# Performance work log

Hardware: AMD Instinct MI355X
Metric: run time of the kernel (lower is better)

The kernel has to match this reference:

```python
import jax, jax.numpy as jnp
import numpy as np

IN_CH, OUT_CH, B, H, W = 32, 64, 8, 256, 256
EPS = 1e-5

SOBEL_X = [[1., 0., -1.], [2., 0., -2.], [1., 0., -1.]]
SOBEL_Y = [[1., 2., 1.], [0., 0., 0.], [-1., -2., -1.]]
LAP = [[0., 1., 0.], [1., -4., 1.], [0., 1., 0.]]

DN = ('NCHW', 'OIHW', 'NCHW')


def conv2d(x, w, b, pad, groups=1):
    y = jax.lax.conv_general_dilated(x, w, (1, 1), [(pad, pad), (pad, pad)],
                                     dimension_numbers=DN, feature_group_count=groups)
    return y + b[None, :, None, None]


def dw_conv(x, k2d):
    # fixed depthwise 3x3 conv, groups=C, padding=1, no bias
    c = x.shape[1]
    kern = jnp.tile(jnp.asarray(k2d, x.dtype)[None, None], (c, 1, 1, 1))  # (C,1,3,3)
    return jax.lax.conv_general_dilated(x, kern, (1, 1), [(1, 1), (1, 1)],
                                        dimension_numbers=DN, feature_group_count=c)


def bn4d(x, p):  # eval-mode BN; x (B,C,H,W), p (4,C) = gamma, beta, mean, var
    g, b, m, v = p
    s = g * jax.lax.rsqrt(v + EPS)
    return (x - m[None, :, None, None]) * s[None, :, None, None] + b[None, :, None, None]


def bn2d(h, p):  # h (B,C)
    g, b, m, v = p
    return (h - m) * (g * jax.lax.rsqrt(v + EPS)) + b


def _bn_params(key, c):
    k1, k2, k3, k4 = jax.random.split(key, 4)
    g = 1.0 + 0.1 * jax.random.normal(k1, (c,), jnp.float32)
    b = 0.1 * jax.random.normal(k2, (c,), jnp.float32)
    m = 0.1 * jax.random.normal(k3, (c,), jnp.float32)
    v = jax.random.uniform(k4, (c,), jnp.float32, 0.5, 1.5)
    return jnp.stack([g, b, m, v])


def setup_inputs() -> dict:
    key = jax.random.key(0)
    ks = jax.random.split(key, 24)
    s = 0.05
    return {
        'x': jax.random.normal(ks[0], (B, IN_CH, H, W), jnp.float32),
        'gate_w1': s * jax.random.normal(ks[1], (IN_CH, IN_CH), jnp.float32),
        'gate_b1': s * jax.random.normal(ks[2], (IN_CH,), jnp.float32),
        'gate_bn': _bn_params(ks[3], IN_CH),
        'gate_w2': s * jax.random.normal(ks[4], (3, IN_CH), jnp.float32),
        'gate_b2': s * jax.random.normal(ks[5], (3,), jnp.float32),
        'mw1': s * jax.random.normal(ks[6], (OUT_CH, IN_CH, 3, 3), jnp.float32),
        'mb1': s * jax.random.normal(ks[7], (OUT_CH,), jnp.float32),
        'mbn1': _bn_params(ks[8], OUT_CH),
        'mw2': s * jax.random.normal(ks[9], (OUT_CH, OUT_CH, 5, 5), jnp.float32),
        'mb2': s * jax.random.normal(ks[10], (OUT_CH,), jnp.float32),
        'mbn2': _bn_params(ks[11], OUT_CH),
        'sxw': s * jax.random.normal(ks[12], (OUT_CH, IN_CH, 5, 5), jnp.float32),
        'sxb': s * jax.random.normal(ks[13], (OUT_CH,), jnp.float32),
        'sxbn': _bn_params(ks[14], OUT_CH),
        'syw': s * jax.random.normal(ks[15], (OUT_CH, IN_CH, 5, 5), jnp.float32),
        'syb': s * jax.random.normal(ks[16], (OUT_CH,), jnp.float32),
        'sybn': _bn_params(ks[17], OUT_CH),
        'lw': s * jax.random.normal(ks[18], (OUT_CH, IN_CH, 5, 5), jnp.float32),
        'lb': s * jax.random.normal(ks[19], (OUT_CH,), jnp.float32),
        'lbn': _bn_params(ks[20], OUT_CH),
    }


def reference(x, gate_w1, gate_b1, gate_bn, gate_w2, gate_b2,
              mw1, mb1, mbn1, mw2, mb2, mbn2,
              sxw, sxb, sxbn, syw, syb, sybn, lw, lb, lbn):
    # gate: GAP -> 1x1 conv -> BN -> tanh -> 1x1 conv -> top-1 one-hot over 3 experts
    gap = x.mean((2, 3))                                   # (B, C_in)
    h = jnp.tanh(bn2d(gap @ gate_w1.T + gate_b1, gate_bn))
    k = h @ gate_w2.T + gate_b2                            # (B, 3)
    oh = jax.nn.one_hot(jnp.argmax(k, axis=1), 3, dtype=x.dtype)  # (B, 3)

    # expert 0: main branch (conv3x3+BN+ReLU -> conv5x5+BN+ReLU)
    main = jax.nn.relu(bn4d(conv2d(x, mw1, mb1, 1), mbn1))
    main = jax.nn.relu(bn4d(conv2d(main, mw2, mb2, 2), mbn2))

    # expert 1: mean of sobel-x and sobel-y branches
    sx = jax.nn.relu(bn4d(conv2d(dw_conv(x, SOBEL_X), sxw, sxb, 2), sxbn))
    sy = jax.nn.relu(bn4d(conv2d(dw_conv(x, SOBEL_Y), syw, syb, 2), sybn))
    sobel = (sx + sy) * 0.5

    # expert 2: laplacian branch
    lap = jax.nn.relu(bn4d(conv2d(dw_conv(x, LAP), lw, lb, 2), lbn))

    # one-hot gated combination (== stack + one_hot mask + sum in the original)
    w = oh[:, :, None, None, None]  # (B, 3, 1, 1, 1)
    return main * w[:, 0] + sobel * w[:, 1] + lap * w[:, 2]
```

## Files before the change

### kernel.cpp

```cpp
#include <hip/hip_runtime.h>

#define BB 8
#define IC 32
#define OC 64
#define HH 256
#define WW 256
#define EPS 1e-5f

typedef __attribute__((ext_vector_type(8))) short bf16x8;
typedef __attribute__((ext_vector_type(4))) float f32x4;

#define YSTR 40
#define XSTR 40

#define WS_GAP   0
#define WS_BIDX  256
#define WS_W1F   264
#define WS_B1F   (WS_W1F + 9216)
#define WS_W2F   (WS_B1F + 64)
#define WS_B2F   (WS_W2F + 51200)
#define WS_SXWT  (WS_B2F + 64)
#define WS_SXBF  (WS_SXWT + 51200)
#define WS_SYWT  (WS_SXBF + 64)
#define WS_SYBF  (WS_SYWT + 51200)
#define WS_LWT   (WS_SYBF + 64)
#define WS_LBF   (WS_LWT + 51200)
#define WS_XT    (WS_LBF + 64)
#define WS_ZPAD  (WS_XT + 8388608)
#define WS_NEED_FAST ((size_t)(WS_ZPAD + 16) * 4)

__device__ inline unsigned short bf16r(float f) {
    unsigned int u = __float_as_uint(f);
    unsigned int r = (u + 0x7fffu + ((u >> 16) & 1u)) >> 16;
    return (unsigned short)r;
}

__device__ __forceinline__ void gld16(const void* g, const void* l) {
    __builtin_amdgcn_global_load_lds(
        (const __attribute__((address_space(1))) void*)(unsigned long long)(g),
        (__attribute__((address_space(3))) void*)(unsigned int)(unsigned long long)(l),
        16, 0, 0);
}

__global__ void prep_kernel(const float* __restrict__ mw1, const float* __restrict__ mb1, const float* __restrict__ mbn1,
                            const float* __restrict__ mw2, const float* __restrict__ mb2, const float* __restrict__ mbn2,
                            const float* __restrict__ sxw, const float* __restrict__ sxb, const float* __restrict__ sxbn,
                            const float* __restrict__ syw, const float* __restrict__ syb, const float* __restrict__ sybn,
                            const float* __restrict__ lw,  const float* __restrict__ lb,  const float* __restrict__ lbn,
                            float* __restrict__ ws, int fast) {
    int idx = blockIdx.x * 256 + threadIdx.x;

    if (idx < 18432) {
        int j = idx & 7, lane = (idx >> 3) & 63, oct = (idx >> 9) & 1, ht = idx >> 10;
        int t = ht % 9, h = ht / 9;
        int oc = h * 32 + oct * 16 + (lane & 15);
        int ic = (lane >> 4) * 8 + j;
        float s = mbn1[oc] * rsqrtf(mbn1[192 + oc] + EPS);
        ((unsigned short*)(ws + WS_W1F))[idx] = bf16r(mw1[(oc * IC + ic) * 9 + t] * s);
    }
    if (idx < 102400) {
        int j = idx & 7, lane = (idx >> 3) & 63, oct = (idx >> 9) & 3, ht = idx >> 11;
        int t = ht % 25, h = ht / 25;
        int oc = oct * 16 + (lane & 15);
        int ic = h * 32 + (lane >> 4) * 8 + j;
        float s = mbn2[oc] * rsqrtf(mbn2[192 + oc] + EPS);
        ((unsigned short*)(ws + WS_W2F))[idx] = bf16r(mw2[(oc * OC + ic) * 25 + t] * s);
    }
    if (idx < 51200) {
        int oc = idx & 63, k = (idx >> 6) % 25, ic = idx / (25 * 64);
        float ssx = sxbn[oc] * rsqrtf(sxbn[192 + oc] + EPS);
        float ssy = sybn[oc] * rsqrtf(sybn[192 + oc] + EPS);
        float sl  = lbn[oc]  * rsqrtf(lbn[192 + oc]  + EPS);
        ws[WS_SXWT + idx] = sxw[(oc * IC + ic) * 25 + k] * ssx;
        ws[WS_SYWT + idx] = syw[(oc * IC + ic) * 25 + k] * ssy;
        ws[WS_LWT  + idx] = lw [(oc * IC + ic) * 25 + k] * sl;
    }
    if (idx < 256) ws[WS_GAP + idx] = 0.f;
    if (fast && idx < 16) ws[WS_ZPAD + idx] = 0.f;
    if (idx < 64) {
        float s1 = mbn1[idx] * rsqrtf(mbn1[192 + idx] + EPS);
        ws[WS_B1F + idx] = (mb1[idx] - mbn1[128 + idx]) * s1 + mbn1[64 + idx];
        float s2 = mbn2[idx] * rsqrtf(mbn2[192 + idx] + EPS);
        ws[WS_B2F + idx] = (mb2[idx] - mbn2[128 + idx]) * s2 + mbn2[64 + idx];
        float sx = sxbn[idx] * rsqrtf(sxbn[192 + idx] + EPS);
        ws[WS_SXBF + idx] = (sxb[idx] - sxbn[128 + idx]) * sx + sxbn[64 + idx];
        float sy = sybn[idx] * rsqrtf(sybn[192 + idx] + EPS);
        ws[WS_SYBF + idx] = (syb[idx] - sybn[128 + idx]) * sy + sybn[64 + idx];
        float sl = lbn[idx] * rsqrtf(lbn[192 + idx] + EPS);
        ws[WS_LBF + idx] = (lb[idx] - lbn[128 + idx]) * sl + lbn[64 + idx];
    }
}

__global__ void __launch_bounds__(256, 2)
xform_kernel(const float* __restrict__ x, float* __restrict__ ws) {
    int b = blockIdx.y, row = blockIdx.x, t = threadIdx.x;
    const float* xb = x + (size_t)b * (IC * HH * WW) + (size_t)row * WW;

    unsigned int pk[16];
    #pragma unroll
    for (int k = 0; k < 32; k += 2) {
        float v0 = xb[(size_t)k * (HH * WW) + t];
        float v1 = xb[(size_t)(k + 1) * (HH * WW) + t];
        pk[k >> 1] = (unsigned int)bf16r(v0) | ((unsigned int)bf16r(v1) << 16);
    }
    short* xt = (short*)(ws + WS_XT) + ((size_t)b * (HH * WW) + (size_t)row * WW + t) * 32;
    uint4* dp = (uint4*)xt;
    dp[0] = make_uint4(pk[0],  pk[1],  pk[2],  pk[3]);
    dp[1] = make_uint4(pk[4],  pk[5],  pk[6],  pk[7]);
    dp[2] = make_uint4(pk[8],  pk[9],  pk[10], pk[11]);
    dp[3] = make_uint4(pk[12], pk[13], pk[14], pk[15]);

    __shared__ float gl[32];
    int w = t >> 6, lane = t & 63;
    #pragma unroll
    for (int kk = 0; kk < 8; kk++) {
        int k = w * 8 + kk;
        const float* rp = xb + (size_t)k * (HH * WW);
        float s = rp[lane] + rp[lane + 64] + rp[lane + 128] + rp[lane + 192];
        #pragma unroll
        for (int off = 32; off; off >>= 1) s += __shfl_down(s, off, 64);
        if (lane == 0) gl[k] = s;
    }
    __syncthreads();
    if (t < 32) atomicAdd(ws + WS_GAP + b * 32 + t, gl[t] * (1.f / (HH * WW)));
}

__global__ void gap_kernel(const float* __restrict__ x, float* __restrict__ ws) {
    int bc = blockIdx.x;
    const float4* p = (const float4*)(x + (size_t)bc * (HH * WW));
    float s = 0.f;
    for (int i = threadIdx.x; i < (HH * WW) / 4; i += 256) {
        float4 v = p[i];
        s += (v.x + v.y) + (v.z + v.w);
    }
    #pragma unroll
    for (int off = 32; off; off >>= 1) s += __shfl_down(s, off, 64);
    __shared__ float red[4];
    int lane = threadIdx.x & 63, w = threadIdx.x >> 6;
    if (lane == 0) red[w] = s;
    __syncthreads();
    if (threadIdx.x == 0)
        ws[WS_GAP + bc] = (red[0] + red[1] + red[2] + red[3]) * (1.f / (HH * WW));
}

__global__ void gate_kernel(const float* __restrict__ w1, const float* __restrict__ b1,
                            const float* __restrict__ gbn,
                            const float* __restrict__ w2, const float* __restrict__ b2,
                            float* __restrict__ ws) {
    __shared__ float hsh[8][32];
    int tid = threadIdx.x;
    int b = tid >> 5, j = tid & 31;
    float acc = b1[j];
    for (int i = 0; i < 32; i++) acc += ws[WS_GAP + b * 32 + i] * w1[j * 32 + i];
    float s = gbn[j] * rsqrtf(gbn[96 + j] + EPS);
    hsh[b][j] = tanhf((acc - gbn[64 + j]) * s + gbn[32 + j]);
    __syncthreads();
    if (tid < 8) {
        float best = -1e30f; int bi = 0;
        for (int c = 0; c < 3; c++) {
            float k = b2[c];
            for (int jj = 0; jj < 32; jj++) k += hsh[tid][jj] * w2[c * 32 + jj];
            if (k > best) { best = k; bi = c; }
        }
        ((int*)ws)[WS_BIDX + tid] = bi;
    }
}

template <int ASYNC>
__global__ void __launch_bounds__(256, 2)
main_kernel(const float* __restrict__ x, const float* __restrict__ ws, float* __restrict__ out) {
    __shared__ __align__(1024) short xs[ASYNC ? 496 * 32 : 484 * XSTR];
    __shared__ __align__(16)   short ys[400 * YSTR];

    int b = blockIdx.y;
    if (((const int*)ws)[WS_BIDX + b] != 0) return;
    int tile = blockIdx.x;
    int ty = (tile >> 4) * 16, tx = (tile & 15) * 16;
    int tid = threadIdx.x;
    int w = tid >> 6, lane = tid & 63, n = lane & 15, quad = lane >> 4;

    if constexpr (ASYNC) {
        const short* xtb = (const short*)(ws + WS_XT) + (size_t)b * (HH * WW * 32);
        const void* zp = (const void*)(ws + WS_ZPAD);
        for (int c = w; c < 31; c += 4) {
            int D = c * 1024 + (lane << 4);
            int L = D ^ (((D >> 7) & 7) << 4);
            int pL = L >> 6, qL = (L >> 4) & 3;
            int rr = pL / 22, cc2 = pL - rr * 22;
            int gy = ty - 3 + rr, gx = tx - 3 + cc2;
            bool v = (pL < 484) && ((unsigned)gy < HH) && ((unsigned)gx < WW);
            const void* src = v ? (const void*)(xtb + (((gy << 8) + gx) * 32) + (qL << 3)) : zp;
            gld16(src, (const void*)((const char*)xs + c * 1024));
        }
    } else {
        const float* xb = x + (size_t)b * IC * HH * WW;
        for (int p = tid; p < 484; p += 256) {
            int rr = p / 22, cc = p % 22;
            int gy = ty - 3 + rr, gx = tx - 3 + cc;
            bool v = ((unsigned)gy < HH) && ((unsigned)gx < WW);
            const float* xp = xb + gy * WW + gx;
            short* dst = xs + p * XSTR;
            #pragma unroll
            for (int ic = 0; ic < IC; ic += 4) {
                float f0 = v ? xp[(size_t)(ic + 0) * (HH * WW)] : 0.f;
                float f1 = v ? xp[(size_t)(ic + 1) * (HH * WW)] : 0.f;
                float f2 = v ? xp[(size_t)(ic + 2) * (HH * WW)] : 0.f;
                float f3 = v ? xp[(size_t)(ic + 3) * (HH * WW)] : 0.f;
                uint2 pk;
                pk.x = (unsigned int)bf16r(f0) | ((unsigned int)bf16r(f1) << 16);
                pk.y = (unsigned int)bf16r(f2) | ((unsigned int)bf16r(f3) << 16);
                *(uint2*)(dst + ic) = pk;
            }
        }
    }

    auto ldb = [&](int P) -> bf16x8 {
        if constexpr (ASYNC) {
            int L = (P << 6) + (quad << 4);
            int A = L ^ (((L >> 7) & 7) << 4);
            return *(const bf16x8*)((const char*)xs + A);
        } else {
            return *(const bf16x8*)(xs + P * XSTR + quad * 8);
        }
    };

    const short* w1v = (const short*)(ws + WS_W1F);
    const bf16x8* w2v = (const bf16x8*)(ws + WS_W2F);

    f32x4 acc2[4][4];
    #pragma unroll
    for (int i = 0; i < 4; i++)
        #pragma unroll
        for (int jj = 0; jj < 4; jj++) acc2[i][jj] = (f32x4){0.f, 0.f, 0.f, 0.f};
    int mrow0 = w * 4;
    int yr0   = w * 5;

    __syncthreads();

    #pragma unroll 1
    for (int h = 0; h < 2; h++) {
        if (h) __syncthreads();

        #pragma unroll
        for (int cg = 0; cg < 2; cg++) {
            int cb = cg * 4;
            f32x4 a1[5][2];
            #pragma unroll
            for (int rr = 0; rr < 5; rr++) {
                a1[rr][0] = (f32x4){0.f, 0.f, 0.f, 0.f};
                a1[rr][1] = (f32x4){0.f, 0.f, 0.f, 0.f};
            }
            #pragma unroll
            for (int dw = 0; dw < 3; dw++) {
                bf16x8 w1f[3][2];
                #pragma unroll
                for (int dh = 0; dh < 3; dh++) {
                    int t = dh * 3 + dw;
                    w1f[dh][0] = *(const bf16x8*)(w1v + (((h * 9 + t) * 2 + 0) * 64 + lane) * 8);
                    w1f[dh][1] = *(const bf16x8*)(w1v + (((h * 9 + t) * 2 + 1) * 64 + lane) * 8);
                }
                bf16x8 bfr[7];
                #pragma unroll
                for (int rI = 0; rI < 7; rI++)
                    bfr[rI] = ldb((yr0 + rI) * 22 + cb + n + dw);
                #pragma unroll
                for (int dh = 0; dh < 3; dh++)
                    #pragma unroll
                    for (int rr = 0; rr < 5; rr++) {
                        a1[rr][0] = __builtin_amdgcn_mfma_f32_16x16x32_bf16(w1f[dh][0], bfr[rr + dh], a1[rr][0], 0, 0, 0);
                        a1[rr][1] = __builtin_amdgcn_mfma_f32_16x16x32_bf16(w1f[dh][1], bfr[rr + dh], a1[rr][1], 0, 0, 0);
                    }
            }
            #pragma unroll
            for (int oct = 0; oct < 2; oct++) {
                float bias1[4];
                #pragma unroll
                for (int r = 0; r < 4; r++)
                    bias1[r] = ws[WS_B1F + h * 32 + oct * 16 + quad * 4 + r];
                #pragma unroll
                for (int rr = 0; rr < 5; rr++) {
                    int yr = yr0 + rr;
                    int gy2 = ty - 2 + yr, gx2 = tx - 2 + cb + n;
                    bool inb = ((unsigned)gy2 < HH) && ((unsigned)gx2 < WW);
                    float v0 = inb ? fmaxf(a1[rr][oct][0] + bias1[0], 0.f) : 0.f;
                    float v1 = inb ? fmaxf(a1[rr][oct][1] + bias1[1], 0.f) : 0.f;
                    float v2 = inb ? fmaxf(a1[rr][oct][2] + bias1[2], 0.f) : 0.f;
                    float v3 = inb ? fmaxf(a1[rr][oct][3] + bias1[3], 0.f) : 0.f;
                    uint2 pkk;
                    pkk.x = (unsigned int)bf16r(v0) | ((unsigned int)bf16r(v1) << 16);
                    pkk.y = (unsigned int)bf16r(v2) | ((unsigned int)bf16r(v3) << 16);
                    *(uint2*)(ys + (yr * 20 + cb + n) * YSTR + oct * 16 + quad * 4) = pkk;
                }
            }
        }
        __syncthreads();

        const bf16x8* w2h = w2v + (size_t)h * 100 * 64;
        bf16x8 afq[4][4];
        #pragma unroll
        for (int kp = 0; kp < 4; kp++) {
            int tn = (kp % 5) * 5 + (kp / 5);
            int base = tn * 256 + lane;
            afq[kp][0] = w2h[base];       afq[kp][1] = w2h[base + 64];
            afq[kp][2] = w2h[base + 128]; afq[kp][3] = w2h[base + 192];
        }
        bf16x8 bfr2[8];
        #pragma unroll
        for (int k = 0; k < 25; k++) {
            int dw = k / 5, dh = k % 5;
            if (dh == 0) {
                #pragma unroll
                for (int rI = 0; rI < 8; rI++)
                    bfr2[rI] = *(const bf16x8*)(ys + ((mrow0 + rI) * 20 + n + dw) * YSTR + quad * 8);
            }
            #pragma unroll
            for (int r4 = 0; r4 < 4; r4++) {
                bf16x8 bb = bfr2[r4 + dh];
                acc2[r4][0] = __builtin_amdgcn_mfma_f32_16x16x32_bf16(afq[k & 3][0], bb, acc2[r4][0], 0, 0, 0);
                acc2[r4][1] = __builtin_amdgcn_mfma_f32_16x16x32_bf16(afq[k & 3][1], bb, acc2[r4][1], 0, 0, 0);
                acc2[r4][2] = __builtin_amdgcn_mfma_f32_16x16x32_bf16(afq[k & 3][2], bb, acc2[r4][2], 0, 0, 0);
                acc2[r4][3] = __builtin_amdgcn_mfma_f32_16x16x32_bf16(afq[k & 3][3], bb, acc2[r4][3], 0, 0, 0);
            }
            if (k + 4 < 25) {
                int kk = k + 4;
                int tn = (kk % 5) * 5 + (kk / 5);
                int base = tn * 256 + lane;
                afq[k & 3][0] = w2h[base];       afq[k & 3][1] = w2h[base + 64];
                afq[k & 3][2] = w2h[base + 128]; afq[k & 3][3] = w2h[base + 192];
            }
        }
    }

    float bias2[4][4];
    #pragma unroll
    for (int oct = 0; oct < 4; oct++)
        #pragma unroll
        for (int r = 0; r < 4; r++)
            bias2[oct][r] = ws[WS_B2F + oct * 16 + quad * 4 + r];

    float* ob = out + (size_t)b * OC * HH * WW;
    #pragma unroll
    for (int r4 = 0; r4 < 4; r4++) {
        int orow = mrow0 + r4;
        #pragma unroll
        for (int oct = 0; oct < 4; oct++) {
            #pragma unroll
            for (int r = 0; r < 4; r++) {
                int oc = oct * 16 + quad * 4 + r;
                float v = fmaxf(acc2[r4][oct][r] + bias2[oct][r], 0.f);
                ob[(size_t)oc * (HH * WW) + (ty + orow) * WW + tx + n] = v;
            }
        }
    }
}

__global__ void __launch_bounds__(256, 2)
edge_kernel(const float* __restrict__ x, const float* __restrict__ ws, float* __restrict__ out) {
    constexpr float KSX[9] = {1, 0, -1, 2, 0, -2, 1, 0, -1};
    constexpr float KSY[9] = {1, 2, 1, 0, 0, 0, -1, -2, -1};
    constexpr float KLP[9] = {0, 1, 0, 1, -4, 1, 0, 1, 0};

    __shared__ float xsf[8 * 484];
    __shared__ float ysf[8 * 400];
    int b = blockIdx.y;
    int sel = ((const int*)ws)[WS_BIDX + b];
    if (sel == 0) return;
    int npass = (sel == 1) ? 2 : 1;
    float scale = (sel == 1) ? 0.5f : 1.0f;

    int tile = blockIdx.x;
    int ty = (tile >> 4) * 16, tx = (tile & 15) * 16;
    int tid = threadIdx.x;
    const float* xb = x + (size_t)b * IC * HH * WW;

    int ocg = tid >> 5;
    int ps  = tid & 31;
    int row = ps >> 1, c0 = (ps & 1) * 8;

    for (int pass = 0; pass < npass; pass++) {
        int kid = (sel == 1) ? pass : 2;
        const float* wt = ws + (kid == 0 ? WS_SXWT : (kid == 1 ? WS_SYWT : WS_LWT));
        const float* bf = ws + (kid == 0 ? WS_SXBF : (kid == 1 ? WS_SYBF : WS_LBF));

        float acc[8][8];
        #pragma unroll
        for (int o = 0; o < 8; o++)
            #pragma unroll
            for (int j = 0; j < 8; j++) acc[o][j] = 0.f;

        for (int icc = 0; icc < 4; icc++) {
            if (icc || pass) __syncthreads();
            for (int i = tid; i < 8 * 484; i += 256) {
                int ch = i / 484, rem = i % 484, rr = rem / 22, cc = rem % 22;
                int ic = icc * 8 + ch;
                int gy = ty - 3 + rr, gx = tx - 3 + cc;
                float v = 0.f;
                if ((unsigned)gy < HH && (unsigned)gx < WW) v = xb[(size_t)ic * HH * WW + gy * WW + gx];
                xsf[i] = v;
            }
            __syncthreads();
            for (int p = tid; p < 400; p += 256) {
                int r = p / 20, c = p % 20;
                bool inb = ((unsigned)(ty - 2 + r) < HH) && ((unsigned)(tx - 2 + c) < WW);
                #pragma unroll
                for (int ch = 0; ch < 8; ch++) {
                    const float* xp = xsf + ch * 484 + r * 22 + c;
                    float v = 0.f;
                    #pragma unroll
                    for (int k = 0; k < 9; k++) {
                        float kv = (kid == 0) ? KSX[k] : (kid == 1) ? KSY[k] : KLP[k];
                        v += kv * xp[(k / 3) * 22 + (k % 3)];
                    }
                    ysf[ch * 400 + p] = inb ? v : 0.f;
                }
            }
            __syncthreads();
            for (int ic8 = 0; ic8 < 8; ic8++) {
                const float* yc = ysf + ic8 * 400;
                const float* wbase = wt + ((icc * 8 + ic8) * 25) * 64 + ocg * 8;
                #pragma unroll
                for (int dh = 0; dh < 5; dh++) {
                    #pragma unroll
                    for (int dw = 0; dw < 5; dw++) {
                        const float* yp = yc + (row + dh) * 20 + c0 + dw;
                        float yv[8];
                        #pragma unroll
                        for (int j = 0; j < 8; j++) yv[j] = yp[j];
                        const float4* wp = (const float4*)(wbase + (dh * 5 + dw) * 64);
                        float4 wa = wp[0], wb = wp[1];
                        float wr[8] = {wa.x, wa.y, wa.z, wa.w, wb.x, wb.y, wb.z, wb.w};
                        #pragma unroll
                        for (int o = 0; o < 8; o++)
                            #pragma unroll
                            for (int j = 0; j < 8; j++) acc[o][j] += wr[o] * yv[j];
                    }
                }
            }
        }
        float* ob = out + (size_t)b * OC * HH * WW;
        #pragma unroll
        for (int o = 0; o < 8; o++) {
            int oc = ocg * 8 + o;
            float bb = bf[oc];
            float* op = ob + (size_t)oc * HH * WW + (ty + row) * WW + tx + c0;
            if (pass) {
                #pragma unroll
                for (int j = 0; j < 8; j++) op[j] += scale * fmaxf(acc[o][j] + bb, 0.f);
            } else {
                #pragma unroll
                for (int j = 0; j < 8; j++) op[j] = scale * fmaxf(acc[o][j] + bb, 0.f);
            }
        }
    }
}

extern "C" void kernel_launch(void* const* d_in, const int* in_sizes, int n_in,
                              void* d_out, int out_size, void* d_ws, size_t ws_size,
                              hipStream_t stream) {
    const float* x    = (const float*)d_in[0];
    const float* gw1  = (const float*)d_in[1];
    const float* gb1  = (const float*)d_in[2];
    const float* gbn  = (const float*)d_in[3];
    const float* gw2  = (const float*)d_in[4];
    const float* gb2  = (const float*)d_in[5];
    const float* mw1  = (const float*)d_in[6];
    const float* mb1  = (const float*)d_in[7];
    const float* mbn1 = (const float*)d_in[8];
    const float* mw2  = (const float*)d_in[9];
    const float* mb2  = (const float*)d_in[10];
    const float* mbn2 = (const float*)d_in[11];
    const float* sxw  = (const float*)d_in[12];
    const float* sxb  = (const float*)d_in[13];
    const float* sxbn = (const float*)d_in[14];
    const float* syw  = (const float*)d_in[15];
    const float* syb  = (const float*)d_in[16];
    const float* sybn = (const float*)d_in[17];
    const float* lw   = (const float*)d_in[18];
    const float* lb   = (const float*)d_in[19];
    const float* lbn  = (const float*)d_in[20];
    float* ws  = (float*)d_ws;
    float* out = (float*)d_out;

    int fast = (ws_size >= WS_NEED_FAST) ? 1 : 0;

    prep_kernel<<<400, 256, 0, stream>>>(mw1, mb1, mbn1, mw2, mb2, mbn2,
                                         sxw, sxb, sxbn, syw, syb, sybn, lw, lb, lbn, ws, fast);
    if (fast) {
        xform_kernel<<<dim3(HH, BB), 256, 0, stream>>>(x, ws);
    } else {
        gap_kernel<<<256, 256, 0, stream>>>(x, ws);
    }
    gate_kernel<<<1, 256, 0, stream>>>(gw1, gb1, gbn, gw2, gb2, ws);

    dim3 grid(256, BB);
    if (fast) {
        main_kernel<1><<<grid, 256, 0, stream>>>(x, ws, out);
    } else {
        main_kernel<0><<<grid, 256, 0, stream>>>(x, ws, out);
    }
    edge_kernel<<<grid, 256, 0, stream>>>(x, ws, out);
}
```

Measured before the change: 435.4 us.

## Port edge-expert conv5x5 to bf16 MFMA with async transposed input staging

Rewrites the edge (sobel/laplacian) kernel so its 5x5 conv runs on bf16 MFMA instructions instead of scalar FP32 FMAs. Weights are pre-packed in prep as bf16 in MFMA fragment order. The input tile comes from the pre-transposed bf16 channels-last workspace via async global-to-LDS loads with swizzling. All 32 channels are staged at once, and both sobel passes are accumulated in registers before a single store, which removes the read-modify-write of the output. The cost is lower precision (bf16 inputs, depthwise results and weights) and higher register use for the two accumulator sets.

```diff
diff --git a/kernel.cpp b/kernel.cpp
--- a/kernel.cpp
+++ b/kernel.cpp
@@ -34,6 +34,9 @@
     unsigned int r = (u + 0x7fffu + ((u >> 16) & 1u)) >> 16;
     return (unsigned short)r;
 }
+__device__ inline float bf2f(unsigned short s) {
+    return __uint_as_float(((unsigned int)s) << 16);
+}
 
 __device__ __forceinline__ void gld16(const void* g, const void* l) {
     __builtin_amdgcn_global_load_lds(
@@ -67,13 +70,15 @@
         ((unsigned short*)(ws + WS_W2F))[idx] = bf16r(mw2[(oc * OC + ic) * 25 + t] * s);
     }
     if (idx < 51200) {
-        int oc = idx & 63, k = (idx >> 6) % 25, ic = idx / (25 * 64);
+        int j = idx & 7, lane = (idx >> 3) & 63, oct = (idx >> 9) & 3, t = idx >> 11;
+        int oc = oct * 16 + (lane & 15);
+        int ic = (lane >> 4) * 8 + j;
         float ssx = sxbn[oc] * rsqrtf(sxbn[192 + oc] + EPS);
         float ssy = sybn[oc] * rsqrtf(sybn[192 + oc] + EPS);
         float sl  = lbn[oc]  * rsqrtf(lbn[192 + oc]  + EPS);
-        ws[WS_SXWT + idx] = sxw[(oc * IC + ic) * 25 + k] * ssx;
-        ws[WS_SYWT + idx] = syw[(oc * IC + ic) * 25 + k] * ssy;
-        ws[WS_LWT  + idx] = lw [(oc * IC + ic) * 25 + k] * sl;
+        ((unsigned short*)(ws + WS_SXWT))[idx] = bf16r(sxw[(oc * IC + ic) * 25 + t] * ssx);
+        ((unsigned short*)(ws + WS_SYWT))[idx] = bf16r(syw[(oc * IC + ic) * 25 + t] * ssy);
+        ((unsigned short*)(ws + WS_LWT ))[idx] = bf16r(lw [(oc * IC + ic) * 25 + t] * sl);
     }
     if (idx < 256) ws[WS_GAP + idx] = 0.f;
     if (fast && idx < 16) ws[WS_ZPAD + idx] = 0.f;
@@ -354,101 +359,176 @@
     }
 }
 
+template <int ASYNC>
 __global__ void __launch_bounds__(256, 2)
 edge_kernel(const float* __restrict__ x, const float* __restrict__ ws, float* __restrict__ out) {
     constexpr float KSX[9] = {1, 0, -1, 2, 0, -2, 1, 0, -1};
     constexpr float KSY[9] = {1, 2, 1, 0, 0, 0, -1, -2, -1};
     constexpr float KLP[9] = {0, 1, 0, 1, -4, 1, 0, 1, 0};
 
-    __shared__ float xsf[8 * 484];
-    __shared__ float ysf[8 * 400];
+    __shared__ __align__(1024) short xs[ASYNC ? 496 * 32 : 484 * XSTR];
+    __shared__ __align__(16)   short ys[400 * YSTR];
+
     int b = blockIdx.y;
     int sel = ((const int*)ws)[WS_BIDX + b];
     if (sel == 0) return;
-    int npass = (sel == 1) ? 2 : 1;
-    float scale = (sel == 1) ? 0.5f : 1.0f;
-
     int tile = blockIdx.x;
     int ty = (tile >> 4) * 16, tx = (tile & 15) * 16;
     int tid = threadIdx.x;
-    const float* xb = x + (size_t)b * IC * HH * WW;
-
-    int ocg = tid >> 5;
-    int ps  = tid & 31;
-    int row = ps >> 1, c0 = (ps & 1) * 8;
-
+    int w = tid >> 6, lane = tid & 63, n = lane & 15, quad = lane >> 4;
+
+    if constexpr (ASYNC) {
+        const short* xtb = (const short*)(ws + WS_XT) + (size_t)b * (HH * WW * 32);
+        const void* zp = (const void*)(ws + WS_ZPAD);
+        for (int c = w; c < 31; c += 4) {
+            int D = c * 1024 + (lane << 4);
+            int L = D ^ (((D >> 7) & 7) << 4);
+            int pL = L >> 6, qL = (L >> 4) & 3;
+            int rr = pL / 22, cc2 = pL - rr * 22;
+            int gy = ty - 3 + rr, gx = tx - 3 + cc2;
+            bool v = (pL < 484) && ((unsigned)gy < HH) && ((unsigned)gx < WW);
+            const void* src = v ? (const void*)(xtb + (((gy << 8) + gx) * 32) + (qL << 3)) : zp;
+            gld16(src, (const void*)((const char*)xs + c * 1024));
+        }
+    } else {
+        const float* xb = x + (size_t)b * IC * HH * WW;
+        for (int p = tid; p < 484; p += 256) {
+            int rr = p / 22, cc = p % 22;
+            int gy = ty - 3 + rr, gx = tx - 3 + cc;
+            bool v = ((unsigned)gy < HH) && ((unsigned)gx < WW);
+            const float* xp = xb + gy * WW + gx;
+            short* dst = xs + p * XSTR;
+            #pragma unroll
+            for (int ic = 0; ic < IC; ic += 4) {
+                float f0 = v ? xp[(size_t)(ic + 0) * (HH * WW)] : 0.f;
+                float f1 = v ? xp[(size_t)(ic + 1) * (HH * WW)] : 0.f;
+                float f2 = v ? xp[(size_t)(ic + 2) * (HH * WW)] : 0.f;
+                float f3 = v ? xp[(size_t)(ic + 3) * (HH * WW)] : 0.f;
+                uint2 pk;
+                pk.x = (unsigned int)bf16r(f0) | ((unsigned int)bf16r(f1) << 16);
+                pk.y = (unsigned int)bf16r(f2) | ((unsigned int)bf16r(f3) << 16);
+                *(uint2*)(dst + ic) = pk;
+            }
+        }
+    }
+
+    auto ldq = [&](int P, int q) -> bf16x8 {
+        if constexpr (ASYNC) {
+            int L = (P << 6) + (q << 4);
+            int A = L ^ (((L >> 7) & 7) << 4);
+            return *(const bf16x8*)((const char*)xs + A);
+        } else {
+            return *(const bf16x8*)(xs + P * XSTR + q * 8);
+        }
+    };
+
+    int mrow0 = w * 4;
+    int npass = (sel == 1) ? 2 : 1;
+    f32x4 accA[4][4];
+    f32x4 acc2[4][4];
+
+    __syncthreads();
+
+    #pragma unroll 1
     for (int pass = 0; pass < npass; pass++) {
         int kid = (sel == 1) ? pass : 2;
-        const float* wt = ws + (kid == 0 ? WS_SXWT : (kid == 1 ? WS_SYWT : WS_LWT));
-        const float* bf = ws + (kid == 0 ? WS_SXBF : (kid == 1 ? WS_SYBF : WS_LBF));
-
-        float acc[8][8];
-        #pragma unroll
-        for (int o = 0; o < 8; o++)
-            #pragma unroll
-            for (int j = 0; j < 8; j++) acc[o][j] = 0.f;
-
-        for (int icc = 0; icc < 4; icc++) {
-            if (icc || pass) __syncthreads();
-            for (int i = tid; i < 8 * 484; i += 256) {
-                int ch = i / 484, rem = i % 484, rr = rem / 22, cc = rem % 22;
-                int ic = icc * 8 + ch;
-                int gy = ty - 3 + rr, gx = tx - 3 + cc;
-                float v = 0.f;
-                if ((unsigned)gy < HH && (unsigned)gx < WW) v = xb[(size_t)ic * HH * WW + gy * WW + gx];
-                xsf[i] = v;
-            }
-            __syncthreads();
-            for (int p = tid; p < 400; p += 256) {
-                int r = p / 20, c = p % 20;
-                bool inb = ((unsigned)(ty - 2 + r) < HH) && ((unsigned)(tx - 2 + c) < WW);
-                #pragma unroll
-                for (int ch = 0; ch < 8; ch++) {
-                    const float* xp = xsf + ch * 484 + r * 22 + c;
-                    float v = 0.f;
+        if (pass) __syncthreads();
+
+        for (int t2 = tid; t2 < 1600; t2 += 256) {
+            int q = t2 & 3, px = t2 >> 2;
+            int pr = px / 20, pc = px - pr * 20;
+            bool inb = ((unsigned)(ty - 2 + pr) < HH) && ((unsigned)(tx - 2 + pc) < WW);
+            float a[8] = {0.f, 0.f, 0.f, 0.f, 0.f, 0.f, 0.f, 0.f};
+            if (inb) {
+                #pragma unroll
+                for (int dr = 0; dr < 3; dr++)
                     #pragma unroll
-                    for (int k = 0; k < 9; k++) {
-                        float kv = (kid == 0) ? KSX[k] : (kid == 1) ? KSY[k] : KLP[k];
-                        v += kv * xp[(k / 3) * 22 + (k % 3)];
+                    for (int dc = 0; dc < 3; dc++) {
+                        float kv = (kid == 0) ? KSX[dr * 3 + dc]
+                                 : (kid == 1) ? KSY[dr * 3 + dc]
+                                              : KLP[dr * 3 + dc];
+                        if (kv != 0.f) {
+                            bf16x8 v = ldq((pr + dr) * 22 + pc + dc, q);
+                            #pragma unroll
+                            for (int j = 0; j < 8; j++)
+                                a[j] += kv * bf2f((unsigned short)v[j]);
+                        }
                     }
-                    ysf[ch * 400 + p] = inb ? v : 0.f;
+            }
+            uint4 pk;
+            pk.x = (unsigned int)bf16r(a[0]) | ((unsigned int)bf16r(a[1]) << 16);
+            pk.y = (unsigned int)bf16r(a[2]) | ((unsigned int)bf16r(a[3]) << 16);
+            pk.z = (unsigned int)bf16r(a[4]) | ((unsigned int)bf16r(a[5]) << 16);
+            pk.w = (unsigned int)bf16r(a[6]) | ((unsigned int)bf16r(a[7]) << 16);
+            *(uint4*)(ys + px * YSTR + q * 8) = pk;
+        }
+        __syncthreads();
+
+        #pragma unroll
+        for (int i = 0; i < 4; i++)
+            #pragma unroll
+            for (int jj = 0; jj < 4; jj++) acc2[i][jj] = (f32x4){0.f, 0.f, 0.f, 0.f};
+
+        const bf16x8* wf = (const bf16x8*)(ws + (kid == 0 ? WS_SXWT : kid == 1 ? WS_SYWT : WS_LWT));
+        bf16x8 afq[2][4];
+        #pragma unroll
+        for (int kp = 0; kp < 2; kp++) {
+            int tn = kp * 5;
+            int base = tn * 256 + lane;
+            afq[kp][0] = wf[base];       afq[kp][1] = wf[base + 64];
+            afq[kp][2] = wf[base + 128]; afq[kp][3] = wf[base + 192];
+        }
+        bf16x8 bfr2[8];
+        #pragma unroll
+        for (int k = 0; k < 25; k++) {
+            int dw = k / 5, dh = k % 5;
+            if (dh == 0) {
+                #pragma unroll
+                for (int rI = 0; rI < 8; rI++)
+                    bfr2[rI] = *(const bf16x8*)(ys + ((mrow0 + rI) * 20 + n + dw) * YSTR + quad * 8);
+            }
+            #pragma unroll
+            for (int r4 = 0; r4 < 4; r4++) {
+                bf16x8 bb = bfr2[r4 + dh];
+                acc2[r4][0] = __builtin_amdgcn_mfma_f32_16x16x32_bf16(afq[k & 1][0], bb, acc2[r4][0], 0, 0, 0);
+                acc2[r4][1] = __builtin_amdgcn_mfma_f32_16x16x32_bf16(afq[k & 1][1], bb, acc2[r4][1], 0, 0, 0);
+                acc2[r4][2] = __builtin_amdgcn_mfma_f32_16x16x32_bf16(afq[k & 1][2], bb, acc2[r4][2], 0, 0, 0);
+                acc2[r4][3] = __builtin_amdgcn_mfma_f32_16x16x32_bf16(afq[k & 1][3], bb, acc2[r4][3], 0, 0, 0);
+            }
+            if (k + 2 < 25) {
+                int kk = k + 2;
+                int tn = (kk % 5) * 5 + (kk / 5);
+                int base = tn * 256 + lane;
+                afq[k & 1][0] = wf[base];       afq[k & 1][1] = wf[base + 64];
+                afq[k & 1][2] = wf[base + 128]; afq[k & 1][3] = wf[base + 192];
+            }
+        }
+        if (sel == 1 && pass == 0) {
+            #pragma unroll
+            for (int i = 0; i < 4; i++)
+                #pragma unroll
+                for (int jj = 0; jj < 4; jj++) accA[i][jj] = acc2[i][jj];
+        }
+    }
+
+    float* ob = out + (size_t)b * OC * HH * WW;
+    #pragma unroll
+    for (int r4 = 0; r4 < 4; r4++) {
+        int orow = mrow0 + r4;
+        #pragma unroll
+        for (int oct = 0; oct < 4; oct++) {
+            #pragma unroll
+            for (int r = 0; r < 4; r++) {
+                int oc = oct * 16 + quad * 4 + r;
+                float v;
+                if (sel == 1) {
+                    float vx = fmaxf(accA[r4][oct][r] + ws[WS_SXBF + oc], 0.f);
+                    float vy = fmaxf(acc2[r4][oct][r] + ws[WS_SYBF + oc], 0.f);
+                    v = 0.5f * (vx + vy);
+                } else {
+                    v = fmaxf(acc2[r4][oct][r] + ws[WS_LBF + oc], 0.f);
                 }
-            }
-            __syncthreads();
-            for (int ic8 = 0; ic8 < 8; ic8++) {
-                const float* yc = ysf + ic8 * 400;
-                const float* wbase = wt + ((icc * 8 + ic8) * 25) * 64 + ocg * 8;
-                #pragma unroll
-                for (int dh = 0; dh < 5; dh++) {
-                    #pragma unroll
-                    for (int dw = 0; dw < 5; dw++) {
-                        const float* yp = yc + (row + dh) * 20 + c0 + dw;
-                        float yv[8];
-                        #pragma unroll
-                        for (int j = 0; j < 8; j++) yv[j] = yp[j];
-                        const float4* wp = (const float4*)(wbase + (dh * 5 + dw) * 64);
-                        float4 wa = wp[0], wb = wp[1];
-                        float wr[8] = {wa.x, wa.y, wa.z, wa.w, wb.x, wb.y, wb.z, wb.w};
-                        #pragma unroll
-                        for (int o = 0; o < 8; o++)
-                            #pragma unroll
-                            for (int j = 0; j < 8; j++) acc[o][j] += wr[o] * yv[j];
-                    }
-                }
-            }
-        }
-        float* ob = out + (size_t)b * OC * HH * WW;
-        #pragma unroll
-        for (int o = 0; o < 8; o++) {
-            int oc = ocg * 8 + o;
-            float bb = bf[oc];
-            float* op = ob + (size_t)oc * HH * WW + (ty + row) * WW + tx + c0;
-            if (pass) {
-                #pragma unroll
-                for (int j = 0; j < 8; j++) op[j] += scale * fmaxf(acc[o][j] + bb, 0.f);
-            } else {
-                #pragma unroll
-                for (int j = 0; j < 8; j++) op[j] = scale * fmaxf(acc[o][j] + bb, 0.f);
+                ob[(size_t)oc * (HH * WW) + (ty + orow) * WW + tx + n] = v;
             }
         }
     }
@@ -495,8 +575,9 @@
     dim3 grid(256, BB);
     if (fast) {
         main_kernel<1><<<grid, 256, 0, stream>>>(x, ws, out);
+        edge_kernel<1><<<grid, 256, 0, stream>>>(x, ws, out);
     } else {
         main_kernel<0><<<grid, 256, 0, stream>>>(x, ws, out);
-    }
-    edge_kernel<<<grid, 256, 0, stream>>>(x, ws, out);
-}
+        edge_kernel<0><<<grid, 256, 0, stream>>>(x, ws, out);
+    }
+}
```

After: 435.7 us. No clear change (+0.1%).
